# Kernel optimization log

Measured on AMD Instinct MI355X. Metric: run time of the kernel, lower is better.

Reference implementation:

```python
import jax, jax.numpy as jnp
import numpy as np
import math

HIDDEN = 2048
NUM_HEADS = 16
NUM_KV_HEADS = 4
HEAD_DIM = 128
GROUPS = NUM_HEADS // NUM_KV_HEADS
BATCH = 1
SEQ = 4096
THETA = 10000.0


def _rope(x):
    # x: [B, h, S, D], interleaved-pair rotation as in the torch module
    seq = x.shape[2]
    freqs = 1.0 / (THETA ** (jnp.arange(0, HEAD_DIM, 2, dtype=jnp.float32) / HEAD_DIM))  # [D/2]
    angles = jnp.arange(seq, dtype=jnp.float32)[:, None] * freqs[None, :]  # [S, D/2]
    cos = jnp.cos(angles)[None, None]  # [1,1,S,D/2]
    sin = jnp.sin(angles)[None, None]
    x1 = x[..., 0::2]
    x2 = x[..., 1::2]
    # stack along new last axis then flatten -> interleaved layout
    rot = jnp.stack([x1 * cos - x2 * sin, x1 * sin + x2 * cos], axis=-1)
    return rot.reshape(x.shape)


def setup_inputs() -> dict:
    key = jax.random.key(0)
    kx, kq, kk, kv, ko = jax.random.split(key, 5)
    scale = 0.02
    x = jax.random.normal(kx, (BATCH, SEQ, HIDDEN), dtype=jnp.float32)
    Wq = jax.random.normal(kq, (NUM_HEADS * HEAD_DIM, HIDDEN), dtype=jnp.float32) * scale
    Wk = jax.random.normal(kk, (NUM_KV_HEADS * HEAD_DIM, HIDDEN), dtype=jnp.float32) * scale
    Wv = jax.random.normal(kv, (NUM_KV_HEADS * HEAD_DIM, HIDDEN), dtype=jnp.float32) * scale
    Wo = jax.random.normal(ko, (HIDDEN, NUM_HEADS * HEAD_DIM), dtype=jnp.float32) * scale
    return {"x": x, "Wq": Wq, "Wk": Wk, "Wv": Wv, "Wo": Wo}


def reference(x, Wq, Wk, Wv, Wo):
    B, S, _ = x.shape
    q = (x @ Wq.T).reshape(B, S, NUM_HEADS, HEAD_DIM).transpose(0, 2, 1, 3)      # [B,16,S,D]
    k = (x @ Wk.T).reshape(B, S, NUM_KV_HEADS, HEAD_DIM).transpose(0, 2, 1, 3)   # [B,4,S,D]
    v = (x @ Wv.T).reshape(B, S, NUM_KV_HEADS, HEAD_DIM).transpose(0, 2, 1, 3)
    q = _rope(q)
    k = _rope(k)
    # GQA: repeat_interleave KV heads across the group dim
    k = jnp.repeat(k, GROUPS, axis=1)  # [B,16,S,D]
    v = jnp.repeat(v, GROUPS, axis=1)
    scale = 1.0 / math.sqrt(HEAD_DIM)
    scores = jnp.einsum("bhqd,bhkd->bhqk", q, k) * scale  # [B,16,S,S]
    causal = jnp.triu(jnp.ones((S, S), dtype=bool), k=1)
    scores = jnp.where(causal[None, None], jnp.float32(-jnp.inf), scores)
    attn = jax.nn.softmax(scores, axis=-1)
    out = jnp.einsum("bhqk,bhkd->bhqd", attn, v)           # [B,16,S,D]
    out = out.transpose(0, 2, 1, 3).reshape(B, S, NUM_HEADS * HEAD_DIM)
    return out @ Wo.T
```

## Files before the change

### kernel.cpp

```cpp
#include <hip/hip_runtime.h>
#include <hip/hip_bf16.h>

typedef unsigned short u16;
typedef unsigned int u32;
typedef short short8 __attribute__((ext_vector_type(8)));
typedef unsigned short ushort4v __attribute__((ext_vector_type(4)));
typedef float f32x4 __attribute__((ext_vector_type(4)));
typedef float f32x16 __attribute__((ext_vector_type(16)));
typedef u32 u32x4 __attribute__((ext_vector_type(4)));

#define SEQN 4096
#define HID 2048
#define NH 16
#define NKV 4
#define HD 128
#define QDIM 2048
#define KVD 512
#define QKVS 3072

static __device__ __forceinline__ float bf2f(u16 u){
  unsigned x = ((unsigned)u) << 16; float f; __builtin_memcpy(&f, &x, 4); return f;
}
static __device__ __forceinline__ u16 f2bf(float f){
  unsigned x; __builtin_memcpy(&x, &f, 4);
  x += 0x7fffu + ((x >> 16) & 1u);
  return (u16)(x >> 16);
}
static __device__ __forceinline__ u32 pk2(float a, float b){
  return (u32)f2bf(a) | ((u32)f2bf(b) << 16);
}

#define G1 (SEQN*HID/4)
#define G2 (QDIM*HID/4)
#define G3 (KVD*HID/4)
#define G4 (KVD*HID/4)
#define G5 (HID*QDIM/4)
__global__ __launch_bounds__(256) void cvt5_kernel(const float* __restrict__ x,  const float* __restrict__ Wq,
                                                   const float* __restrict__ Wk, const float* __restrict__ Wv,
                                                   const float* __restrict__ Wo, u16* __restrict__ xb,
                                                   u16* __restrict__ Wqkvb, u16* __restrict__ Wob){
  int g = blockIdx.x * 256 + threadIdx.x;
  const float* src; u16* dst; int off;
  if (g < G1)                { src = x;  dst = xb;    off = g; }
  else if (g < G1+G2)        { src = Wq; dst = Wqkvb; off = g - G1; }
  else if (g < G1+G2+G3)     { src = Wk; dst = Wqkvb + (size_t)QDIM*HID;        off = g - (G1+G2); }
  else if (g < G1+G2+G3+G4)  { src = Wv; dst = Wqkvb + (size_t)(QDIM+KVD)*HID;  off = g - (G1+G2+G3); }
  else if (g < G1+G2+G3+G4+G5){ src = Wo; dst = Wob;  off = g - (G1+G2+G3+G4); }
  else return;
  f32x4 v = ((const f32x4*)src)[off];
  ushort4v o;
  o.x = f2bf(v.x); o.y = f2bf(v.y); o.z = f2bf(v.z); o.w = f2bf(v.w);
  ((ushort4v*)dst)[off] = o;
}

__global__ __launch_bounds__(256) void rope2_kernel(u16* __restrict__ QKVb){
  int idx = blockIdx.x * 256 + threadIdx.x;
  if (idx >= SEQN * (NH + NKV) * 16) return;
  int i8 = idx & 15;
  int rest = idx >> 4;
  int h = rest % (NH + NKV);
  int s = rest / (NH + NKV);
  int col = (h < NH) ? h * HD : QDIM + (h - NH) * HD;
  u16* p = QKVb + (size_t)s * QKVS + col + i8 * 8;
  short8 v = *(const short8*)p;
  short8 o;
#pragma unroll
  for (int j = 0; j < 4; j++){
    int i = i8 * 4 + j;
    float freq = expf(-0.14391156831212788f * (float)i);
    float ang = (float)s * freq;
    float c = cosf(ang), sn = sinf(ang);
    float x1 = bf2f((u16)v[2*j]), x2 = bf2f((u16)v[2*j+1]);
    o[2*j]   = (short)f2bf(x1 * c - x2 * sn);
    o[2*j+1] = (short)f2bf(x1 * sn + x2 * c);
  }
  *(short8*)p = o;
}

__global__ __launch_bounds__(256) void vtrans_kernel(const u16* __restrict__ V, int vstride, u16* __restrict__ VTg){
  __shared__ u16 T[64][72];
  const int s0 = blockIdx.x * 64;
  const int c0 = blockIdx.y * 64;
  const int tid = threadIdx.x;
  const int sl = tid & 63, ch = tid >> 6;
  const u16* src = V + (size_t)(s0 + sl) * vstride + c0 + ch * 16;
  *(short8*)&T[sl][ch * 16]     = *(const short8*)(src);
  *(short8*)&T[sl][ch * 16 + 8] = *(const short8*)(src + 8);
  __syncthreads();
#pragma unroll
  for (int it = 0; it < 16; it++){
    int c = it * 4 + ch;
    VTg[(size_t)(c0 + c) * SEQN + s0 + sl] = T[sl][c];
  }
}

static __device__ __forceinline__ void gload16(const void* g, void* l){
  __builtin_amdgcn_global_load_lds((const __attribute__((address_space(1))) void*)g,
                                   (__attribute__((address_space(3))) void*)l, 16, 0, 0);
}

template<int F32OUT>
__global__ __launch_bounds__(256) void gemm_kernel(const u16* __restrict__ A, const u16* __restrict__ B,
                                                   void* __restrict__ Cout, int M, int N, int Kd, int ldc){
  __shared__ alignas(16) u16 sh[8192];
  u16* As = sh;
  u16* Bs = sh + 4096;
  const int tid = threadIdx.x;
  const int w = tid >> 6, l = tid & 63;
  const int wr = w >> 1, wc = w & 1;
  const int lc = l & 15, lg = l >> 4;
  const int tm = blockIdx.x * 128, tn = blockIdx.y * 128;

  const int srow = w * 32 + (l >> 2);
  const int scol = (l & 3) * 8;
  const u16* Ag = A + (size_t)(tm + srow) * Kd + scol;
  const u16* Bg = B + (size_t)(tn + srow) * Kd + scol;
  u16* As0 = As + (w * 2) * 512;
  u16* Bs0 = Bs + (w * 2) * 512;

  f32x4 acc[4][4] = {};

  for (int k0 = 0; k0 < Kd; k0 += 32){
    gload16(Ag + k0,                    As0);
    gload16(Ag + k0 + (size_t)16 * Kd,  As0 + 512);
    gload16(Bg + k0,                    Bs0);
    gload16(Bg + k0 + (size_t)16 * Kd,  Bs0 + 512);
    __syncthreads();
    short8 a[4], b[4];
#pragma unroll
    for (int mi = 0; mi < 4; mi++) a[mi] = *(const short8*)&As[(wr*64 + mi*16 + lc) * 32 + lg*8];
#pragma unroll
    for (int ni = 0; ni < 4; ni++) b[ni] = *(const short8*)&Bs[(wc*64 + ni*16 + lc) * 32 + lg*8];
#pragma unroll
    for (int mi = 0; mi < 4; mi++)
#pragma unroll
      for (int ni = 0; ni < 4; ni++)
        acc[mi][ni] = __builtin_amdgcn_mfma_f32_16x16x32_bf16(a[mi], b[ni], acc[mi][ni], 0, 0, 0);
    __syncthreads();
  }

  if (F32OUT){
#pragma unroll
    for (int mi = 0; mi < 4; mi++)
#pragma unroll
      for (int ni = 0; ni < 4; ni++)
#pragma unroll
        for (int r = 0; r < 4; r++){
          int row = tm + wr*64 + mi*16 + lg*4 + r;
          int col = tn + wc*64 + ni*16 + lc;
          ((float*)Cout)[(size_t)row * ldc + col] = acc[mi][ni][r];
        }
  } else {
    __syncthreads();
    u16* Ew = sh + w * 1168;
#pragma unroll
    for (int mi = 0; mi < 4; mi++){
#pragma unroll
      for (int ni = 0; ni < 4; ni++)
#pragma unroll
        for (int r = 0; r < 4; r++)
          Ew[(lg * 4 + r) * 73 + ni * 16 + lc] = f2bf(acc[mi][ni][r]);
#pragma unroll
      for (int pass = 0; pass < 2; pass++){
        int row = pass * 8 + (l >> 3);
        short8 v;
#pragma unroll
        for (int j = 0; j < 8; j++) v[j] = (short)Ew[row * 73 + (l & 7) * 8 + j];
        *(short8*)((u16*)Cout + (size_t)(tm + wr*64 + mi*16 + row) * ldc + tn + wc*64 + (l & 7) * 8) = v;
      }
    }
  }
}

__global__ __launch_bounds__(256, 2) void attn_kernel(const u16* __restrict__ Qg, const u16* __restrict__ Kgb,
                                                      const u16* __restrict__ VTg, u16* __restrict__ Aout,
                                                      u16* __restrict__ PO, float* __restrict__ mP,
                                                      float* __restrict__ LP){
  __shared__ alignas(16) char pool[65536];

  const int pr  = blockIdx.x;
  const int h   = blockIdx.y;
  const int s   = blockIdx.z;
  const int kvh = h >> 2;
  const int tid = threadIdx.x;
  const int w = tid >> 6, l = tid & 63;
  const int q5 = l & 31;
  const int hi = l >> 5;
  const int hi4 = hi * 4;
  const float csc = 0.12751743f;

  const u16* Ksrc[4];
  const u16* Vsrc[4];
#pragma unroll
  for (int i = 0; i < 4; i++){
    int blk = w * 4 + i;
    int row = blk * 4 + (l >> 4);
    int cg  = (l & 15) ^ (row & 15);
    Ksrc[i] = Kgb + (size_t)row * QKVS + kvh * HD + cg * 8;
    int d   = blk * 8 + (l >> 3);
    int cv  = (l & 7) ^ (d & 7);
    Vsrc[i] = VTg + (size_t)(kvh * 128 + d) * SEQN + cv * 8;
  }

  auto issueTile = [&](int b, int kv0){
    char* Ksb = pool + b * 32768;
    char* VTb = Ksb + 16384;
#pragma unroll
    for (int i = 0; i < 4; i++)
      gload16(Ksrc[i] + (size_t)kv0 * QKVS, Ksb + (w * 4 + i) * 1024);
#pragma unroll
    for (int i = 0; i < 4; i++)
      gload16(Vsrc[i] + kv0, VTb + (w * 4 + i) * 1024);
  };

  const int qlo = pr, qhi = 31 - pr;
  int nseg, sq[2], st0[2], st1[2], smode[2];
  if (s == 0){
    nseg = 2;
    sq[0] = qlo; st0[0] = 0;           st1[0] = 2 * pr + 2;   smode[0] = 0;
    sq[1] = qhi; st0[1] = 0;           st1[1] = 31 - 2 * pr;  smode[1] = 1;
  } else {
    nseg = 1;
    sq[0] = qhi; st0[0] = 31 - 2 * pr; st1[0] = 64 - 2 * pr;  smode[0] = 2;
  }

  for (int sg = 0; sg < nseg; sg++){
    const int qt = sq[sg], t0 = st0[sg], t1 = st1[sg], mode = smode[sg];
    const int qbase = qt * 128 + w * 32;
    const int qa    = qbase + q5;

    short8 qf[8];
    {
      const u16* qp = Qg + (size_t)(qbase + q5) * QKVS + h * HD + hi * 8;
#pragma unroll
      for (int k0 = 0; k0 < 8; k0++) qf[k0] = *(const short8*)(qp + k0 * 16);
    }

    f32x16 Ov[4] = {};
    float Lrow = 0.f;
    float ms = -1e30f;

    auto computeTile = [&](int b, int kv0){
      if (kv0 > qbase + 31) return;
      char* Ksb = pool + b * 32768;
      char* VTb = Ksb + 16384;
      f32x16 Sv[2] = {};
#pragma unroll
      for (int k0 = 0; k0 < 8; k0++){
#pragma unroll
        for (int nb = 0; nb < 2; nb++){
          int kvr = nb * 32 + q5;
          short8 kf = *(const short8*)(Ksb + kvr * 256 + (((k0 * 2 + hi) ^ (kvr & 15)) << 4));
          Sv[nb] = __builtin_amdgcn_mfma_f32_32x32x16_bf16(kf, qf[k0], Sv[nb], 0, 0, 0);
        }
      }
      if (kv0 + 63 > qbase){
#pragma unroll
        for (int nb = 0; nb < 2; nb++)
#pragma unroll
          for (int r = 0; r < 16; r++){
            int kva = kv0 + nb * 32 + (r & 3) + 8 * (r >> 2) + hi4;
            if (kva > qa) Sv[nb][r] = -1e30f;
          }
      }
      float tm = -3e38f;
#pragma unroll
      for (int nb = 0; nb < 2; nb++)
#pragma unroll
        for (int r = 0; r < 16; r++) tm = fmaxf(tm, Sv[nb][r]);
      tm = fmaxf(tm, __shfl_xor(tm, 32));
      float tms = tm * csc;
      if (!__all(tms - ms <= 8.f)){
        float nms = fmaxf(ms, tms);
        float al = __builtin_amdgcn_exp2f(ms - nms);
        ms = nms;
        Lrow *= al;
#pragma unroll
        for (int nb = 0; nb < 4; nb++)
#pragma unroll
          for (int r = 0; r < 16; r++) Ov[nb][r] *= al;
      }
      float ts = 0.f;
#pragma unroll
      for (int nb = 0; nb < 2; nb++)
#pragma unroll
        for (int r = 0; r < 16; r++){
          float p = __builtin_amdgcn_exp2f(__builtin_fmaf(Sv[nb][r], csc, -ms));
          Sv[nb][r] = p;
          ts += p;
        }
      ts += __shfl_xor(ts, 32);
      Lrow += ts;
#pragma unroll
      for (int kc = 0; kc < 4; kc++){
        const int nb = kc >> 1, rb = (kc & 1) * 8;
        u32 Aw = pk2(Sv[nb][rb + 0], Sv[nb][rb + 1]);
        u32 Bw = pk2(Sv[nb][rb + 2], Sv[nb][rb + 3]);
        u32 Cw = pk2(Sv[nb][rb + 4], Sv[nb][rb + 5]);
        u32 Dw = pk2(Sv[nb][rb + 6], Sv[nb][rb + 7]);
        u32 sAw = __shfl_xor(Aw, 32);
        u32 sBw = __shfl_xor(Bw, 32);
        u32 sCw = __shfl_xor(Cw, 32);
        u32 sDw = __shfl_xor(Dw, 32);
        u32 w0 = hi ? sCw : Aw;
        u32 w1 = hi ? sDw : Bw;
        u32 w2 = hi ? Cw : sAw;
        u32 w3 = hi ? Dw : sBw;
        u32x4 pw4 = {w0, w1, w2, w3};
        short8 pf = *(short8*)&pw4;
#pragma unroll
        for (int nbd = 0; nbd < 4; nbd++){
          int drow = nbd * 32 + q5;
          short8 vf = *(const short8*)(VTb + drow * 128 + (((kc * 2 + hi) ^ (drow & 7)) << 4));
          Ov[nbd] = __builtin_amdgcn_mfma_f32_32x32x16_bf16(vf, pf, Ov[nbd], 0, 0, 0);
        }
      }
    };

    __syncthreads();
    issueTile(0, t0 * 64);
    __syncthreads();
    int cur = 0;
    for (int t = t0; t < t1; t++){
      if (t + 1 < t1) issueTile(cur ^ 1, (t + 1) * 64);
      computeTile(cur, t * 64);
      __syncthreads();
      cur ^= 1;
    }

    u16* Ew = (u16*)(pool + w * 8704);
    float rl = (mode == 0) ? (1.f / Lrow) : 1.f;
#pragma unroll
    for (int nbd = 0; nbd < 4; nbd++)
#pragma unroll
      for (int r = 0; r < 16; r += 2){
        int d = nbd * 32 + (r & 3) + 8 * (r >> 2) + hi4;
        u32 wpk = pk2(Ov[nbd][r] * rl, Ov[nbd][r + 1] * rl);
        *(u32*)((char*)Ew + q5 * 272 + d * 2) = wpk;
      }
    if (mode == 0){
#pragma unroll
      for (int pass = 0; pass < 8; pass++){
        int q2 = pass * 4 + (l >> 4);
        short8 ov = *(const short8*)((char*)Ew + q2 * 272 + (l & 15) * 16);
        *(short8*)(Aout + (size_t)(qbase + q2) * QDIM + h * HD + (l & 15) * 8) = ov;
      }
    } else {
      const int p = mode - 1;
      u16* dstb = PO + ((size_t)((p * 16 + pr) * NH + h) * 128) * 128;
#pragma unroll
      for (int pass = 0; pass < 8; pass++){
        int q2 = pass * 4 + (l >> 4);
        short8 ov = *(const short8*)((char*)Ew + q2 * 272 + (l & 15) * 16);
        *(short8*)(dstb + (size_t)(w * 32 + q2) * 128 + (l & 15) * 8) = ov;
      }
      if (hi == 0){
        int idx = ((p * 16 + pr) * NH + h) * 128 + w * 32 + q5;
        mP[idx] = ms;
        LP[idx] = Lrow;
      }
    }
  }
}

__global__ __launch_bounds__(256) void combine_kernel(const u16* __restrict__ PO, const float* __restrict__ mP,
                                                      const float* __restrict__ LP, u16* __restrict__ Aout){
  const int pr = blockIdx.x;
  const int h  = blockIdx.y;
  const int tid = threadIdx.x;
  const int r  = tid >> 1;
  const int dh = (tid & 1) * 64;
  const int qhi = 31 - pr;
  const int idx0 = ((0 * 16 + pr) * NH + h) * 128 + r;
  const int idx1 = ((1 * 16 + pr) * NH + h) * 128 + r;
  float m0 = mP[idx0], m1 = mP[idx1];
  float L0 = LP[idx0], L1 = LP[idx1];
  float M = fmaxf(m0, m1);
  float a0 = __builtin_amdgcn_exp2f(m0 - M);
  float a1 = __builtin_amdgcn_exp2f(m1 - M);
  float rl = 1.f / (L0 * a0 + L1 * a1);
  const u16* o0 = PO + (size_t)idx0 * 128 + dh;
  const u16* o1 = PO + (size_t)idx1 * 128 + dh;
  u16* dst = Aout + (size_t)(qhi * 128 + r) * QDIM + h * HD + dh;
#pragma unroll
  for (int ch = 0; ch < 8; ch++){
    short8 v0 = *(const short8*)(o0 + ch * 8);
    short8 v1 = *(const short8*)(o1 + ch * 8);
    short8 ov;
#pragma unroll
    for (int j = 0; j < 8; j++)
      ov[j] = (short)f2bf((bf2f((u16)v0[j]) * a0 + bf2f((u16)v1[j]) * a1) * rl);
    *(short8*)(dst + ch * 8) = ov;
  }
}

extern "C" void kernel_launch(void* const* d_in, const int* in_sizes, int n_in,
                              void* d_out, int out_size, void* d_ws, size_t ws_size,
                              hipStream_t stream){
  const float* x  = (const float*)d_in[0];
  const float* Wq = (const float*)d_in[1];
  const float* Wk = (const float*)d_in[2];
  const float* Wv = (const float*)d_in[3];
  const float* Wo = (const float*)d_in[4];

  char* p = (char*)d_ws;
  u16* xb    = (u16*)p; p += (size_t)SEQN * HID * 2;
  u16* Wqkvb = (u16*)p; p += (size_t)QKVS * HID * 2;
  u16* Wob   = (u16*)p; p += (size_t)HID * QDIM * 2;
  u16* QKVb  = (u16*)p; p += (size_t)SEQN * QKVS * 2;
  u16* Ab    = (u16*)p; p += (size_t)SEQN * QDIM * 2;
  u16* VTg   = (u16*)p; p += (size_t)SEQN * KVD * 2;
  u16* PO    = (u16*)p; p += (size_t)2 * 16 * NH * 128 * 128 * 2;
  float* mP  = (float*)p; p += (size_t)2 * 16 * NH * 128 * 4;
  float* LP  = (float*)p; p += (size_t)2 * 16 * NH * 128 * 4;

  const int totg = G1 + G2 + G3 + G4 + G5;
  cvt5_kernel<<<(totg + 255) / 256, 256, 0, stream>>>(x, Wq, Wk, Wv, Wo, xb, Wqkvb, Wob);

  gemm_kernel<0><<<dim3(SEQN/128, QKVS/128), 256, 0, stream>>>(xb, Wqkvb, QKVb, SEQN, QKVS, HID, QKVS);

  rope2_kernel<<<(SEQN*(NH+NKV)*16 + 255) / 256, 256, 0, stream>>>(QKVb);

  vtrans_kernel<<<dim3(SEQN/64, KVD/64), 256, 0, stream>>>(QKVb + QDIM + KVD, QKVS, VTg);

  attn_kernel<<<dim3(16, NH, 2), 256, 0, stream>>>(QKVb, QKVb + QDIM, VTg, Ab, PO, mP, LP);
  combine_kernel<<<dim3(16, NH), 256, 0, stream>>>(PO, mP, LP, Ab);

  gemm_kernel<1><<<dim3(SEQN/128, HID/128), 256, 0, stream>>>(Ab, Wob, d_out, SEQN, HID, QDIM, HID);
}
```

Before: 257.5 us.

## Merge rope and V-transpose kernels, use cheaper bf16 rounding, pair softmax reductions

```diff
diff --git a/kernel.cpp b/kernel.cpp
--- a/kernel.cpp
+++ b/kernel.cpp
@@ -26,8 +26,13 @@
   x += 0x7fffu + ((x >> 16) & 1u);
   return (u16)(x >> 16);
 }
-static __device__ __forceinline__ u32 pk2(float a, float b){
-  return (u32)f2bf(a) | ((u32)f2bf(b) << 16);
+static __device__ __forceinline__ u16 f2bfc(float f){
+  unsigned x; __builtin_memcpy(&x, &f, 4);
+  return (u16)((x + 0x8000u) >> 16);
+}
+static __device__ __forceinline__ u32 pkr(float a, float b){
+  u32 ab, bb; __builtin_memcpy(&ab, &a, 4); __builtin_memcpy(&bb, &b, 4);
+  return ((ab + 0x8000u) >> 16) | ((bb + 0x8000u) & 0xffff0000u);
 }
 
 #define G1 (SEQN*HID/4)
@@ -53,44 +58,46 @@
   ((ushort4v*)dst)[off] = o;
 }
 
-__global__ __launch_bounds__(256) void rope2_kernel(u16* __restrict__ QKVb){
-  int idx = blockIdx.x * 256 + threadIdx.x;
-  if (idx >= SEQN * (NH + NKV) * 16) return;
-  int i8 = idx & 15;
-  int rest = idx >> 4;
-  int h = rest % (NH + NKV);
-  int s = rest / (NH + NKV);
-  int col = (h < NH) ? h * HD : QDIM + (h - NH) * HD;
-  u16* p = QKVb + (size_t)s * QKVS + col + i8 * 8;
-  short8 v = *(const short8*)p;
-  short8 o;
-#pragma unroll
-  for (int j = 0; j < 4; j++){
-    int i = i8 * 4 + j;
-    float freq = expf(-0.14391156831212788f * (float)i);
-    float ang = (float)s * freq;
-    float c = cosf(ang), sn = sinf(ang);
-    float x1 = bf2f((u16)v[2*j]), x2 = bf2f((u16)v[2*j+1]);
-    o[2*j]   = (short)f2bf(x1 * c - x2 * sn);
-    o[2*j+1] = (short)f2bf(x1 * sn + x2 * c);
-  }
-  *(short8*)p = o;
-}
-
-__global__ __launch_bounds__(256) void vtrans_kernel(const u16* __restrict__ V, int vstride, u16* __restrict__ VTg){
+#define ROPE_BLKS (SEQN * (NH + NKV) * 16 / 256)
+__global__ __launch_bounds__(256) void prep_kernel(u16* __restrict__ QKVb, u16* __restrict__ VTg){
   __shared__ u16 T[64][72];
-  const int s0 = blockIdx.x * 64;
-  const int c0 = blockIdx.y * 64;
+  const int bid = blockIdx.x;
   const int tid = threadIdx.x;
-  const int sl = tid & 63, ch = tid >> 6;
-  const u16* src = V + (size_t)(s0 + sl) * vstride + c0 + ch * 16;
-  *(short8*)&T[sl][ch * 16]     = *(const short8*)(src);
-  *(short8*)&T[sl][ch * 16 + 8] = *(const short8*)(src + 8);
-  __syncthreads();
-#pragma unroll
-  for (int it = 0; it < 16; it++){
-    int c = it * 4 + ch;
-    VTg[(size_t)(c0 + c) * SEQN + s0 + sl] = T[sl][c];
+  if (bid < ROPE_BLKS){
+    int idx = bid * 256 + tid;
+    int i8 = idx & 15;
+    int rest = idx >> 4;
+    int h = rest % (NH + NKV);
+    int s = rest / (NH + NKV);
+    int col = (h < NH) ? h * HD : QDIM + (h - NH) * HD;
+    u16* p = QKVb + (size_t)s * QKVS + col + i8 * 8;
+    short8 v = *(const short8*)p;
+    short8 o;
+#pragma unroll
+    for (int j = 0; j < 4; j++){
+      int i = i8 * 4 + j;
+      float freq = expf(-0.14391156831212788f * (float)i);
+      float ang = (float)s * freq;
+      float c = cosf(ang), sn = sinf(ang);
+      float x1 = bf2f((u16)v[2*j]), x2 = bf2f((u16)v[2*j+1]);
+      o[2*j]   = (short)f2bfc(x1 * c - x2 * sn);
+      o[2*j+1] = (short)f2bfc(x1 * sn + x2 * c);
+    }
+    *(short8*)p = o;
+  } else {
+    const int b2 = bid - ROPE_BLKS;
+    const int s0 = (b2 & 63) * 64;
+    const int c0 = (b2 >> 6) * 64;
+    const int sl = tid & 63, ch = tid >> 6;
+    const u16* src = QKVb + QDIM + KVD + (size_t)(s0 + sl) * QKVS + c0 + ch * 16;
+    *(short8*)&T[sl][ch * 16]     = *(const short8*)(src);
+    *(short8*)&T[sl][ch * 16 + 8] = *(const short8*)(src + 8);
+    __syncthreads();
+#pragma unroll
+    for (int it = 0; it < 16; it++){
+      int c = it * 4 + ch;
+      VTg[(size_t)(c0 + c) * SEQN + s0 + sl] = T[sl][c];
+    }
   }
 }
 
@@ -159,7 +166,7 @@
       for (int ni = 0; ni < 4; ni++)
 #pragma unroll
         for (int r = 0; r < 4; r++)
-          Ew[(lg * 4 + r) * 73 + ni * 16 + lc] = f2bf(acc[mi][ni][r]);
+          Ew[(lg * 4 + r) * 73 + ni * 16 + lc] = f2bfc(acc[mi][ni][r]);
 #pragma unroll
       for (int pass = 0; pass < 2; pass++){
         int row = pass * 8 + (l >> 3);
@@ -263,11 +270,12 @@
             if (kva > qa) Sv[nb][r] = -1e30f;
           }
       }
-      float tm = -3e38f;
+      float tm = fmaxf(Sv[0][0], Sv[0][1]);
 #pragma unroll
       for (int nb = 0; nb < 2; nb++)
 #pragma unroll
-        for (int r = 0; r < 16; r++) tm = fmaxf(tm, Sv[nb][r]);
+        for (int r = (nb == 0 ? 2 : 0); r < 16; r += 2)
+          tm = fmaxf(tm, fmaxf(Sv[nb][r], Sv[nb][r + 1]));
       tm = fmaxf(tm, __shfl_xor(tm, 32));
       float tms = tm * csc;
       if (!__all(tms - ms <= 8.f)){
@@ -280,24 +288,26 @@
 #pragma unroll
           for (int r = 0; r < 16; r++) Ov[nb][r] *= al;
       }
-      float ts = 0.f;
+      float ts0 = 0.f, ts1 = 0.f;
 #pragma unroll
       for (int nb = 0; nb < 2; nb++)
 #pragma unroll
-        for (int r = 0; r < 16; r++){
-          float p = __builtin_amdgcn_exp2f(__builtin_fmaf(Sv[nb][r], csc, -ms));
-          Sv[nb][r] = p;
-          ts += p;
+        for (int r = 0; r < 16; r += 2){
+          float p0 = __builtin_amdgcn_exp2f(__builtin_fmaf(Sv[nb][r],     csc, -ms));
+          float p1 = __builtin_amdgcn_exp2f(__builtin_fmaf(Sv[nb][r + 1], csc, -ms));
+          Sv[nb][r] = p0; Sv[nb][r + 1] = p1;
+          ts0 += p0; ts1 += p1;
         }
+      float ts = ts0 + ts1;
       ts += __shfl_xor(ts, 32);
       Lrow += ts;
 #pragma unroll
       for (int kc = 0; kc < 4; kc++){
         const int nb = kc >> 1, rb = (kc & 1) * 8;
-        u32 Aw = pk2(Sv[nb][rb + 0], Sv[nb][rb + 1]);
-        u32 Bw = pk2(Sv[nb][rb + 2], Sv[nb][rb + 3]);
-        u32 Cw = pk2(Sv[nb][rb + 4], Sv[nb][rb + 5]);
-        u32 Dw = pk2(Sv[nb][rb + 6], Sv[nb][rb + 7]);
+        u32 Aw = pkr(Sv[nb][rb + 0], Sv[nb][rb + 1]);
+        u32 Bw = pkr(Sv[nb][rb + 2], Sv[nb][rb + 3]);
+        u32 Cw = pkr(Sv[nb][rb + 4], Sv[nb][rb + 5]);
+        u32 Dw = pkr(Sv[nb][rb + 6], Sv[nb][rb + 7]);
         u32 sAw = __shfl_xor(Aw, 32);
         u32 sBw = __shfl_xor(Bw, 32);
         u32 sCw = __shfl_xor(Cw, 32);
@@ -335,7 +345,7 @@
 #pragma unroll
       for (int r = 0; r < 16; r += 2){
         int d = nbd * 32 + (r & 3) + 8 * (r >> 2) + hi4;
-        u32 wpk = pk2(Ov[nbd][r] * rl, Ov[nbd][r + 1] * rl);
+        u32 wpk = pkr(Ov[nbd][r] * rl, Ov[nbd][r + 1] * rl);
         *(u32*)((char*)Ew + q5 * 272 + d * 2) = wpk;
       }
     if (mode == 0){
@@ -386,11 +396,14 @@
   for (int ch = 0; ch < 8; ch++){
     short8 v0 = *(const short8*)(o0 + ch * 8);
     short8 v1 = *(const short8*)(o1 + ch * 8);
-    short8 ov;
-#pragma unroll
-    for (int j = 0; j < 8; j++)
-      ov[j] = (short)f2bf((bf2f((u16)v0[j]) * a0 + bf2f((u16)v1[j]) * a1) * rl);
-    *(short8*)(dst + ch * 8) = ov;
+    u32x4 ow;
+#pragma unroll
+    for (int j = 0; j < 4; j++){
+      float e0 = (bf2f((u16)v0[2*j])   * a0 + bf2f((u16)v1[2*j])   * a1) * rl;
+      float e1 = (bf2f((u16)v0[2*j+1]) * a0 + bf2f((u16)v1[2*j+1]) * a1) * rl;
+      ow[j] = pkr(e0, e1);
+    }
+    *(u32x4*)(dst + ch * 8) = ow;
   }
 }
 
@@ -419,9 +432,7 @@
 
   gemm_kernel<0><<<dim3(SEQN/128, QKVS/128), 256, 0, stream>>>(xb, Wqkvb, QKVb, SEQN, QKVS, HID, QKVS);
 
-  rope2_kernel<<<(SEQN*(NH+NKV)*16 + 255) / 256, 256, 0, stream>>>(QKVb);
-
-  vtrans_kernel<<<dim3(SEQN/64, KVD/64), 256, 0, stream>>>(QKVb + QDIM + KVD, QKVS, VTg);
+  prep_kernel<<<ROPE_BLKS + (SEQN/64) * (KVD/64), 256, 0, stream>>>(QKVb, VTg);
 
   attn_kernel<<<dim3(16, NH, 2), 256, 0, stream>>>(QKVb, QKVb + QDIM, VTg, Ab, PO, mP, LP);
   combine_kernel<<<dim3(16, NH), 256, 0, stream>>>(PO, mP, LP, Ab);
```

After: 254.4 us. No clear change (-1.2%).
